# Kernel optimization log

Measured on AMD Instinct MI355X. Metric: run time of the kernel, lower is better.

Reference implementation:

```python
import jax, jax.numpy as jnp
import numpy as np

B, S, DIM, H, DH, FF = 2, 2048, 2048, 16, 128, 8192
EPS = 1e-6


def rmsnorm(x, g):
    xf = x.astype(jnp.float32)
    y = xf * jax.lax.rsqrt(jnp.mean(xf * xf, axis=-1, keepdims=True) + EPS)
    return y.astype(x.dtype) * g


def rope_cache(seq_len, head_dim):
    inv_freq = 1.0 / (10000.0 ** (jnp.arange(0, head_dim, 2, dtype=jnp.float32) / head_dim))
    t = jnp.arange(seq_len, dtype=jnp.float32)
    freqs = jnp.outer(t, inv_freq)              # [S, DH/2]
    emb = jnp.concatenate([freqs, freqs], -1)   # [S, DH]
    return jnp.cos(emb), jnp.sin(emb)


def rotate_half(x):
    x1, x2 = jnp.split(x, 2, axis=-1)
    return jnp.concatenate([-x2, x1], axis=-1)


def apply_rope(x, cos, sin):
    # x: [B,H,S,DH]; cos/sin: [S,DH] broadcast per position
    c = cos[None, None, :, :]
    s = sin[None, None, :, :]
    return x * c + rotate_half(x) * s


def setup_inputs() -> dict:
    key = jax.random.key(0)
    ks = jax.random.split(key, 10)
    std = 0.02
    x = jax.random.normal(ks[0], (B, S, DIM), jnp.float32)
    mask = jnp.tril(jnp.ones((S, S), dtype=bool))[None, None]  # causal [1,1,S,S]
    wq = jax.random.normal(ks[1], (H * DH, DIM), jnp.float32) * std
    wk = jax.random.normal(ks[2], (H * DH, DIM), jnp.float32) * std
    wv = jax.random.normal(ks[3], (H * DH, DIM), jnp.float32) * std
    wo = jax.random.normal(ks[4], (DIM, H * DH), jnp.float32) * std
    w1 = jax.random.normal(ks[5], (FF, DIM), jnp.float32) * std
    w2 = jax.random.normal(ks[6], (DIM, FF), jnp.float32) * std
    w3 = jax.random.normal(ks[7], (FF, DIM), jnp.float32) * std
    g_attn = jnp.ones((DIM,), jnp.float32)
    g_ffn = jnp.ones((DIM,), jnp.float32)
    return {"x": x, "mask": mask, "wq": wq, "wk": wk, "wv": wv, "wo": wo,
            "w1": w1, "w2": w2, "w3": w3, "g_attn": g_attn, "g_ffn": g_ffn}


def reference(x, mask, wq, wk, wv, wo, w1, w2, w3, g_attn, g_ffn):
    b, s, _ = x.shape
    scale = 1.0 / np.sqrt(DH)
    # --- attention sublayer ---
    h = rmsnorm(x, g_attn)
    q = jnp.einsum('bsd,ed->bse', h, wq).reshape(b, s, H, DH).transpose(0, 2, 1, 3)
    k = jnp.einsum('bsd,ed->bse', h, wk).reshape(b, s, H, DH).transpose(0, 2, 1, 3)
    v = jnp.einsum('bsd,ed->bse', h, wv).reshape(b, s, H, DH).transpose(0, 2, 1, 3)
    cos, sin = rope_cache(s, DH)
    q = apply_rope(q, cos, sin)
    k = apply_rope(k, cos, sin)
    scores = jnp.einsum('bhqd,bhkd->bhqk', q, k) * scale
    scores = jnp.where(mask, scores, -1e9)
    attn = jax.nn.softmax(scores, axis=-1)
    o = jnp.einsum('bhqk,bhkd->bhqd', attn, v)
    o = o.transpose(0, 2, 1, 3).reshape(b, s, H * DH)
    x = x + jnp.einsum('bse,de->bsd', o, wo)
    # --- SwiGLU FFN sublayer ---
    h2 = rmsnorm(x, g_ffn)
    u = jnp.einsum('bsd,fd->bsf', h2, w1)
    g = jnp.einsum('bsd,fd->bsf', h2, w3)
    ff = jnp.einsum('bsf,df->bsd', jax.nn.silu(u) * g, w2)
    return x + ff
```

## Files before the change

kernel.cpp:

```cpp
#include <hip/hip_runtime.h>
#include <hip/hip_bf16.h>
#include <math.h>

typedef __hip_bfloat16 bf16;
typedef short short8 __attribute__((ext_vector_type(8)));
typedef float f32x4 __attribute__((ext_vector_type(4)));

#define Bq 2
#define Sq 2048
#define Dq 2048
#define Hq 16
#define DHq 128
#define FFq 8192
#define Mq 4096

__device__ __forceinline__ float b2f(bf16 x) { return __bfloat162float(x); }
__device__ __forceinline__ bf16 f2b(float x) { return __float2bfloat16(x); }

__device__ __forceinline__ void gload16(const void* g, void* lds_base) {
  __builtin_amdgcn_global_load_lds(
      (const __attribute__((address_space(1))) void*)g,
      (__attribute__((address_space(3))) void*)lds_base,
      16, 0, 0);
}

__global__ __launch_bounds__(256)
void conv_k(const float* __restrict__ src, bf16* __restrict__ dst, long n) {
  const long stride = (long)gridDim.x * 256 * 8;
  for (long i = ((long)blockIdx.x * 256 + threadIdx.x) * 8; i < n; i += stride) {
    f32x4 a = *(const f32x4*)(src + i);
    f32x4 b = *(const f32x4*)(src + i + 4);
    union { short8 s; bf16 h[8]; } u;
#pragma unroll
    for (int j = 0; j < 4; ++j) { u.h[j] = f2b(a[j]); u.h[j + 4] = f2b(b[j]); }
    *(short8*)(dst + i) = u.s;
  }
}

#define BAR8() { asm volatile("" ::: "memory"); __builtin_amdgcn_s_barrier(); asm volatile("" ::: "memory"); }
#define VMC4() { asm volatile("s_waitcnt vmcnt(4)" ::: "memory"); __builtin_amdgcn_sched_barrier(0); }

#define STG8(Gp, ldX, rowOff, kt, XsBuf)                                        \
  gload16(Gp + (size_t)((rowOff) + w8 + lr) * (size_t)(ldX) + (kt) + sCol,      \
          &XsBuf[(rowOff) + w8][0]);                                            \
  gload16(Gp + (size_t)((rowOff) + 64 + w8 + lr) * (size_t)(ldX) + (kt) + sCol, \
          &XsBuf[(rowOff) + 64 + w8][0]);

#define RD_A8(dst, XsBuf, mb)                                                   \
  _Pragma("unroll") for (int mi = 0; mi < 4; ++mi) {                            \
    const int ra = wmBase + ((mb) + mi) * 16 + c;                               \
    _Pragma("unroll") for (int kk = 0; kk < 2; ++kk)                            \
      dst[mi][kk] = *(const short8*)&XsBuf[ra][(((kk * 4 + g) ^ (ra & 7)) << 3)]; \
  }

#define RD_B8(dst, XsBuf, nb_)                                                  \
  _Pragma("unroll") for (int ni = 0; ni < 2; ++ni) {                            \
    const int rb = wnBase + ((nb_) + ni) * 16 + c;                              \
    _Pragma("unroll") for (int kk = 0; kk < 2; ++kk)                            \
      dst[ni][kk] = *(const short8*)&XsBuf[rb][(((kk * 4 + g) ^ (rb & 7)) << 3)]; \
  }

#define MFMA_Q8(afv, bfv, mb, nb_)                                              \
  __builtin_amdgcn_s_setprio(1);                                                \
  _Pragma("unroll") for (int mi = 0; mi < 4; ++mi)                              \
    _Pragma("unroll") for (int ni = 0; ni < 2; ++ni)                            \
      _Pragma("unroll") for (int kk = 0; kk < 2; ++kk)                          \
        acc[(mb) + mi][(nb_) + ni] = __builtin_amdgcn_mfma_f32_16x16x32_bf16(   \
            afv[mi][kk], bfv[ni][kk], acc[(mb) + mi][(nb_) + ni], 0, 0, 0);     \
  __builtin_amdgcn_s_setprio(0);

template <int EPI>
__global__ __launch_bounds__(512, 2)
void gemm8(const bf16* __restrict__ A, const bf16* __restrict__ Bt,
           const void* __restrict__ R, void* __restrict__ C,
           int N, int K, int ldb, long long boff) {
  __shared__ __align__(16) bf16 As[2][256][64];
  __shared__ __align__(16) bf16 Bs[2][256][64];
  const int tid = threadIdx.x;
  const int w = tid >> 6, l = tid & 63;
  const int g = l >> 4, c = l & 15;
  const int w8 = w * 8, lr = l >> 3;
  const int sCol = (((l & 7) ^ lr) << 3);

  const int nwg = gridDim.x * gridDim.y;
  const int orig = blockIdx.x + blockIdx.y * gridDim.x;
  const int qq = nwg >> 3, rr8 = nwg & 7;
  const int xcd = orig & 7, idx8 = orig >> 3;
  const int wg = (xcd < rr8 ? xcd * (qq + 1) : rr8 * (qq + 1) + (xcd - rr8) * qq) + idx8;
  const int bm = (wg / gridDim.x) * 256;
  const int bn = (wg % gridDim.x) * 256;

  const int wmBase = (w >> 2) * 128;
  const int wnBase = (w & 3) * 64;

  const bf16* Ab = A + (size_t)bm * K;
  const bf16* Bb = Bt + (size_t)bn * ldb + (size_t)boff;

  f32x4 acc[8][4] = {};
  const int nt = K >> 6;

  STG8(Ab, K, 0, 0, As[0]); STG8(Ab, K, 128, 0, As[0]);
  STG8(Bb, ldb, 0, 0, Bs[0]); STG8(Bb, ldb, 128, 0, Bs[0]);
  STG8(Bb, ldb, 0, 64, Bs[1]); STG8(Bb, ldb, 128, 64, Bs[1]);
  VMC4(); BAR8();

  short8 af[4][2], af2[4][2], bf[2][2], bf2[2][2];
  for (int it = 0; it < (nt >> 1); ++it) {
    const int t = it * 2;
    const int kt1 = (t + 1) << 6;
    const int kt2 = (t + 2 < nt ? t + 2 : nt - 1) << 6;
    const int kt3 = (t + 3 < nt ? t + 3 : nt - 1) << 6;
    RD_A8(af, As[0], 0); RD_B8(bf, Bs[0], 0); RD_B8(bf2, Bs[0], 2);
    STG8(Ab, K, 0, kt1, As[1]); STG8(Ab, K, 128, kt1, As[1]);
    BAR8();
    MFMA_Q8(af, bf, 0, 0); MFMA_Q8(af, bf2, 0, 2);
    BAR8();
    RD_A8(af2, As[0], 4);
    STG8(Bb, ldb, 0, kt2, Bs[0]); STG8(Bb, ldb, 128, kt2, Bs[0]);
    BAR8();
    MFMA_Q8(af2, bf, 4, 0); MFMA_Q8(af2, bf2, 4, 2);
    VMC4(); BAR8();
    RD_A8(af, As[1], 0); RD_B8(bf, Bs[1], 0); RD_B8(bf2, Bs[1], 2);
    STG8(Ab, K, 0, kt2, As[0]); STG8(Ab, K, 128, kt2, As[0]);
    BAR8();
    MFMA_Q8(af, bf, 0, 0); MFMA_Q8(af, bf2, 0, 2);
    BAR8();
    RD_A8(af2, As[1], 4);
    STG8(Bb, ldb, 0, kt3, Bs[1]); STG8(Bb, ldb, 128, kt3, Bs[1]);
    BAR8();
    MFMA_Q8(af2, bf, 4, 0); MFMA_Q8(af2, bf2, 4, 2);
    VMC4(); BAR8();
  }

  const int rbase = bm + wmBase + g * 4;
  const int cbase = bn + wnBase + c;
#pragma unroll
  for (int m = 0; m < 8; ++m)
#pragma unroll
    for (int r = 0; r < 4; ++r) {
      const int row = rbase + m * 16 + r;
#pragma unroll
      for (int n = 0; n < 4; ++n) {
        const size_t idx = (size_t)row * N + (cbase + n * 16);
        float vacc = acc[m][n][r];
        if (EPI == 1) {
          ((float*)C)[idx] = vacc + ((const float*)R)[idx];
        } else if (EPI == 2) {
          const float u = b2f(((const bf16*)R)[idx]);
          ((bf16*)C)[idx] = f2b((u / (1.f + expf(-u))) * vacc);
        } else {
          ((bf16*)C)[idx] = f2b(vacc);
        }
      }
    }
}

template <int EPI>
__global__ __launch_bounds__(256)
void gemm3(const bf16* __restrict__ A, const bf16* __restrict__ Bt,
           const void* __restrict__ R, void* __restrict__ C,
           int N, int K, int ldb, long long boff) {
  __shared__ __align__(16) bf16 As[128][64];
  __shared__ __align__(16) bf16 Bs[128][64];
  const int tid = threadIdx.x;
  const int w = tid >> 6;
  const int l = tid & 63;

  const int nwg = gridDim.x * gridDim.y;
  const int orig = blockIdx.x + blockIdx.y * gridDim.x;
  const int qq = nwg >> 3, rr8 = nwg & 7;
  const int xcd = orig & 7, idx8 = orig >> 3;
  const int wg = (xcd < rr8 ? xcd * (qq + 1) : rr8 * (qq + 1) + (xcd - rr8) * qq) + idx8;
  const int bm = (wg / gridDim.x) * 128;
  const int bn = (wg % gridDim.x) * 128;

  const int wr = (w >> 1) * 64;
  const int wc = (w & 1) * 64;
  f32x4 acc[4][4] = {};

  const bf16* Ab = A + (size_t)bm * K;
  const bf16* Bb = Bt + (size_t)bn * ldb + (size_t)boff;

  const int sRow = w * 8 + (l >> 3);
  const int sCol = (((l & 7) ^ (l >> 3)) << 3);

  for (int kt = 0; kt < K; kt += 64) {
    __syncthreads();
#pragma unroll
    for (int i = 0; i < 4; ++i) {
      gload16(Ab + (size_t)(i * 32 + sRow) * K + kt + sCol, &As[i * 32 + w * 8][0]);
      gload16(Bb + (size_t)(i * 32 + sRow) * ldb + kt + sCol, &Bs[i * 32 + w * 8][0]);
    }
    __syncthreads();

#pragma unroll
    for (int kk = 0; kk < 2; ++kk) {
      short8 af[4], bfv[4];
#pragma unroll
      for (int m = 0; m < 4; ++m) {
        const int ra = wr + m * 16 + (l & 15);
        af[m] = *(const short8*)&As[ra][(((kk * 4 + (l >> 4)) ^ (ra & 7)) << 3)];
      }
#pragma unroll
      for (int n = 0; n < 4; ++n) {
        const int rb = wc + n * 16 + (l & 15);
        bfv[n] = *(const short8*)&Bs[rb][(((kk * 4 + (l >> 4)) ^ (rb & 7)) << 3)];
      }
#pragma unroll
      for (int m = 0; m < 4; ++m)
#pragma unroll
        for (int n = 0; n < 4; ++n)
          acc[m][n] = __builtin_amdgcn_mfma_f32_16x16x32_bf16(af[m], bfv[n], acc[m][n], 0, 0, 0);
    }
  }

  const int rbase = bm + wr + (l >> 4) * 4;
  const int cbase = bn + wc + (l & 15);
#pragma unroll
  for (int m = 0; m < 4; ++m)
#pragma unroll
    for (int r = 0; r < 4; ++r) {
      const int row = rbase + m * 16 + r;
#pragma unroll
      for (int n = 0; n < 4; ++n) {
        const size_t idx = (size_t)row * N + (cbase + n * 16);
        float vacc = acc[m][n][r];
        if (EPI == 1) {
          ((float*)C)[idx] = vacc + ((const float*)R)[idx];
        } else if (EPI == 2) {
          const float u = b2f(((const bf16*)R)[idx]);
          ((bf16*)C)[idx] = f2b((u / (1.f + expf(-u))) * vacc);
        } else {
          ((bf16*)C)[idx] = f2b(vacc);
        }
      }
    }
}

template <int EPI>
__global__ __launch_bounds__(256)
void gemm2(const bf16* __restrict__ A, const float* __restrict__ Bt,
           const void* __restrict__ R, void* __restrict__ C,
           int N, int K, int ldb, long long boff) {
  __shared__ __align__(16) bf16 As[128][64];
  __shared__ __align__(16) float Bsf[128][64];
  const int tid = threadIdx.x;
  const int w = tid >> 6;
  const int l = tid & 63;

  const int nwg = gridDim.x * gridDim.y;
  const int orig = blockIdx.x + blockIdx.y * gridDim.x;
  const int qq = nwg >> 3, rr8 = nwg & 7;
  const int xcd = orig & 7, idx8 = orig >> 3;
  const int wg = (xcd < rr8 ? xcd * (qq + 1) : rr8 * (qq + 1) + (xcd - rr8) * qq) + idx8;
  const int bm = (wg / gridDim.x) * 128;
  const int bn = (wg % gridDim.x) * 128;

  const int wr = (w >> 1) * 64;
  const int wc = (w & 1) * 64;
  f32x4 acc[4][4] = {};

  const bf16* Ab = A + (size_t)bm * K;
  const float* Bb = Bt + (size_t)bn * ldb + (size_t)boff;

  const int aSrcCol = (((l & 7) ^ (l >> 3)) << 3);
  const int bKey = (w * 4 + (l >> 4)) & 7;
  const int bSrcCol = (((l & 15) ^ bKey) << 2);

  for (int kt = 0; kt < K; kt += 64) {
    __syncthreads();
#pragma unroll
    for (int i = 0; i < 4; ++i)
      gload16(Ab + (size_t)(i * 32 + w * 8 + (l >> 3)) * K + kt + aSrcCol,
              &As[i * 32 + w * 8][0]);
#pragma unroll
    for (int i = 0; i < 8; ++i)
      gload16(Bb + (size_t)(i * 16 + w * 4 + (l >> 4)) * ldb + kt + bSrcCol,
              &Bsf[i * 16 + w * 4][0]);
    __syncthreads();

#pragma unroll
    for (int kk = 0; kk < 2; ++kk) {
      short8 af[4], bfv[4];
#pragma unroll
      for (int m = 0; m < 4; ++m) {
        const int ra = wr + m * 16 + (l & 15);
        const int pb = (kk * 4 + (l >> 4)) ^ (ra & 7);
        af[m] = *(const short8*)&As[ra][pb * 8];
      }
#pragma unroll
      for (int n = 0; n < 4; ++n) {
        const int rb = wc + n * 16 + (l & 15);
        const int b0 = kk * 8 + (l >> 4) * 2;
        const f32x4 x0 = *(const f32x4*)&Bsf[rb][(b0 ^ (rb & 7)) * 4];
        const f32x4 x1 = *(const f32x4*)&Bsf[rb][((b0 + 1) ^ (rb & 7)) * 4];
        union { short8 s; bf16 h[8]; } u;
#pragma unroll
        for (int j = 0; j < 4; ++j) { u.h[j] = f2b(x0[j]); u.h[j + 4] = f2b(x1[j]); }
        bfv[n] = u.s;
      }
#pragma unroll
      for (int m = 0; m < 4; ++m)
#pragma unroll
        for (int n = 0; n < 4; ++n)
          acc[m][n] = __builtin_amdgcn_mfma_f32_16x16x32_bf16(af[m], bfv[n], acc[m][n], 0, 0, 0);
    }
  }

  const int rbase = bm + wr + (l >> 4) * 4;
  const int cbase = bn + wc + (l & 15);
#pragma unroll
  for (int m = 0; m < 4; ++m)
#pragma unroll
    for (int r = 0; r < 4; ++r) {
      const int row = rbase + m * 16 + r;
#pragma unroll
      for (int n = 0; n < 4; ++n) {
        const size_t idx = (size_t)row * N + (cbase + n * 16);
        float vacc = acc[m][n][r];
        if (EPI == 1) {
          ((float*)C)[idx] = vacc + ((const float*)R)[idx];
        } else if (EPI == 2) {
          const float u = b2f(((const bf16*)R)[idx]);
          ((bf16*)C)[idx] = f2b((u / (1.f + expf(-u))) * vacc);
        } else {
          ((bf16*)C)[idx] = f2b(vacc);
        }
      }
    }
}

__global__ __launch_bounds__(256)
void rmsnorm_k(const float* __restrict__ xin, const float* __restrict__ g,
               bf16* __restrict__ out) {
  const int row = blockIdx.x;
  const int tid = threadIdx.x;
  const float* xp = xin + (size_t)row * Dq + tid * 8;
  f32x4 a = *(const f32x4*)xp, b = *(const f32x4*)(xp + 4);
  float xf[8];
#pragma unroll
  for (int j = 0; j < 4; ++j) { xf[j] = a[j]; xf[j + 4] = b[j]; }
  float ss = 0.f;
#pragma unroll
  for (int j = 0; j < 8; ++j) ss += xf[j] * xf[j];
#pragma unroll
  for (int off = 32; off > 0; off >>= 1) ss += __shfl_down(ss, off);
  __shared__ float red[4];
  if ((tid & 63) == 0) red[tid >> 6] = ss;
  __syncthreads();
  const float rms = rsqrtf((red[0] + red[1] + red[2] + red[3]) * (1.f / (float)Dq) + 1e-6f);
  const float* gp = g + tid * 8;
  f32x4 ga = *(const f32x4*)gp, gb = *(const f32x4*)(gp + 4);
  union { short8 s; bf16 h[8]; } uo;
#pragma unroll
  for (int j = 0; j < 4; ++j) {
    uo.h[j] = f2b(xf[j] * rms * ga[j]);
    uo.h[j + 4] = f2b(xf[j + 4] * rms * gb[j]);
  }
  *(short8*)(out + (size_t)row * Dq + tid * 8) = uo.s;
}

__global__ __launch_bounds__(256)
void rope_k(bf16* __restrict__ q, bf16* __restrict__ k, int ld) {
  const size_t idx = (size_t)blockIdx.x * 256 + threadIdx.x;
  const int i = (int)(idx & 63);
  const int h = (int)((idx >> 6) & 15);
  const int s = (int)((idx >> 10) & 2047);
  const int b = (int)(idx >> 21);
  const float f = (float)s * powf(10000.f, -(float)i * (1.f / 64.f));
  float sn, cs;
  sincosf(f, &sn, &cs);
  const size_t base = ((size_t)(b * Sq + s)) * ld + h * DHq + i;
  const float qa = b2f(q[base]), qb_ = b2f(q[base + 64]);
  q[base] = f2b(qa * cs - qb_ * sn);
  q[base + 64] = f2b(qb_ * cs + qa * sn);
  const float ka = b2f(k[base]), kb_ = b2f(k[base + 64]);
  k[base] = f2b(ka * cs - kb_ * sn);
  k[base + 64] = f2b(kb_ * cs + ka * sn);
}

__device__ __forceinline__ int swz8(int row) { return (((row >> 3) ^ row) & 7) << 3; }

#define ATTN_COMPUTE(AQ, QB, QROW, M_, L_, OACC, KV0, CUR)                        \
  {                                                                               \
    f32x4 sc[4] = {};                                                             \
    __builtin_amdgcn_s_setprio(1);                                                \
    _Pragma("unroll") for (int n = 0; n < 4; ++n) {                               \
      const int krow = n * 16 + c;                                                \
      const int sw = swz8(krow);                                                  \
      _Pragma("unroll") for (int kk = 0; kk < 4; ++kk) {                          \
        short8 ak = *(const short8*)&Ks[CUR][krow][(kk * 32 + g * 8) ^ sw];       \
        sc[n] = __builtin_amdgcn_mfma_f32_16x16x32_bf16(ak, AQ[kk], sc[n], 0, 0, 0); \
      }                                                                           \
    }                                                                             \
    __builtin_amdgcn_s_setprio(0);                                                \
    float p[4][4];                                                                \
    float tmax = -3.0e38f;                                                        \
    if ((KV0) + 63 <= (QB)) {                                                     \
      _Pragma("unroll") for (int n = 0; n < 4; ++n)                               \
        _Pragma("unroll") for (int r = 0; r < 4; ++r) {                           \
          const float val = sc[n][r] * SCALE;                                     \
          p[n][r] = val;                                                          \
          tmax = fmaxf(tmax, val);                                                \
        }                                                                         \
    } else {                                                                      \
      _Pragma("unroll") for (int n = 0; n < 4; ++n)                               \
        _Pragma("unroll") for (int r = 0; r < 4; ++r) {                           \
          const int kvg = (KV0) + n * 16 + g * 4 + r;                             \
          float val = sc[n][r] * SCALE;                                           \
          if (kvg > (QROW)) val = -3.0e38f;                                       \
          p[n][r] = val;                                                          \
          tmax = fmaxf(tmax, val);                                                \
        }                                                                         \
    }                                                                             \
    tmax = fmaxf(tmax, __shfl_xor(tmax, 16));                                     \
    tmax = fmaxf(tmax, __shfl_xor(tmax, 32));                                     \
    const bool grow = !__all(tmax <= M_);                                         \
    const float m_new = grow ? fmaxf(M_, tmax) : M_;                              \
    float tsum = 0.f;                                                             \
    _Pragma("unroll") for (int n = 0; n < 4; ++n)                                 \
      _Pragma("unroll") for (int r = 0; r < 4; ++r) {                             \
        const float pv = expf(p[n][r] - m_new);                                   \
        p[n][r] = pv;                                                             \
        tsum += pv;                                                               \
      }                                                                           \
    tsum += __shfl_xor(tsum, 16);                                                 \
    tsum += __shfl_xor(tsum, 32);                                                 \
    if (grow) {                                                                   \
      const float corr = expf(M_ - m_new);                                        \
      L_ = L_ * corr + tsum;                                                      \
      M_ = m_new;                                                                 \
      _Pragma("unroll") for (int dt = 0; dt < 8; ++dt) OACC[dt] *= corr;          \
    } else {                                                                      \
      L_ += tsum;                                                                 \
    }                                                                             \
    const int keyc = (c ^ (c >> 3)) & 7;                                          \
    _Pragma("unroll") for (int n = 0; n < 4; ++n) {                               \
      union { unsigned long long u; bf16 hh[4]; } pk;                             \
      _Pragma("unroll") for (int r = 0; r < 4; ++r) pk.hh[r] = f2b(p[n][r]);      \
      const int blk = (2 * n + (g >> 1)) ^ keyc;                                  \
      *(unsigned long long*)&Ps[w][c][blk * 8 + (g & 1) * 4] = pk.u;              \
    }                                                                             \
    short8 ap[2];                                                                 \
    _Pragma("unroll") for (int kk = 0; kk < 2; ++kk)                              \
      ap[kk] = *(const short8*)&Ps[w][c][(kk * 32 + g * 8) ^ (keyc << 3)];        \
    __builtin_amdgcn_s_setprio(1);                                                \
    _Pragma("unroll") for (int dt = 0; dt < 8; ++dt) {                            \
      const int vrow = dt * 16 + c;                                               \
      const int vsw = swz8(vrow);                                                 \
      _Pragma("unroll") for (int kk = 0; kk < 2; ++kk) {                          \
        short8 av = *(const short8*)&Vt[CUR][vrow][(kk * 32 + g * 8) ^ vsw];      \
        OACC[dt] = __builtin_amdgcn_mfma_f32_16x16x32_bf16(av, ap[kk], OACC[dt], 0, 0, 0); \
      }                                                                           \
    }                                                                             \
    __builtin_amdgcn_s_setprio(0);                                                \
  }

__global__ __launch_bounds__(512)
void attn_k(const bf16* __restrict__ q, const bf16* __restrict__ k,
            const bf16* __restrict__ v, bf16* __restrict__ o, int ld) {
  __shared__ __align__(16) bf16 Ks[2][64][128];
  __shared__ __align__(16) bf16 Vt[2][128][64];
  __shared__ __align__(16) bf16 Ps[8][16][64];
  const int tid = threadIdx.x;
  const int w = tid >> 6, l = tid & 63;
  const int g = l >> 4, c = l & 15;
  const int x = blockIdx.x;
  const int h = blockIdx.y;
  const int b = blockIdx.z;
  const size_t hoff = (size_t)h * DHq;
  const float SCALE = 0.08838834764831845f;

  const int q0h = (15 - x) * 128, q0l = x * 128;
  const int qbh = q0h + w * 16, qbl = q0l + w * 16;
  const int qrh = qbh + c, qrl = qbl + c;

  short8 aqh[4], aql[4];
  {
    const bf16* qph = q + (size_t)(b * Sq + qrh) * ld + hoff + g * 8;
    const bf16* qpl = q + (size_t)(b * Sq + qrl) * ld + hoff + g * 8;
#pragma unroll
    for (int kk = 0; kk < 4; ++kk) {
      aqh[kk] = *(const short8*)(qph + kk * 32);
      aql[kk] = *(const short8*)(qpl + kk * 32);
    }
  }

  float mh = -3.0e38f, lh = 0.f, ml = -3.0e38f, ll_ = 0.f;
  f32x4 oh[8] = {}, ol[8] = {};

  const int stRow = tid >> 4;
  const int stBlk = tid & 15;
  const int ntiles = (q0h >> 6) + 2;

  {
#pragma unroll
    for (int i = 0; i < 2; ++i) {
      const int kr = i * 32 + w * 4 + (l >> 4);
      const int key = (kr ^ (kr >> 3)) & 7;
      gload16(k + (size_t)(b * Sq + kr) * ld + hoff + ((c ^ key) << 3),
              &Ks[0][i * 32 + w * 4][0]);
    }
    const int c0 = stBlk * 8;
#pragma unroll
    for (int i = 0; i < 2; ++i) {
      const int vr = i * 32 + stRow;
      union { short8 s; bf16 hh[8]; } uv;
      uv.s = *(const short8*)(v + (size_t)(b * Sq + vr) * ld + hoff + c0);
#pragma unroll
      for (int j = 0; j < 8; ++j) Vt[0][c0 + j][vr ^ swz8(c0 + j)] = uv.hh[j];
    }
  }
  __syncthreads();

  for (int t = 0; t < ntiles; ++t) {
    const int cur = t & 1, nxt = cur ^ 1;
    const int kv0 = t * 64;
    const bool pf = (t + 1 < ntiles);
    short8 vpa, vpb;
    if (pf) {
      const int kvn = kv0 + 64;
#pragma unroll
      for (int i = 0; i < 2; ++i) {
        const int kr = i * 32 + w * 4 + (l >> 4);
        const int key = (kr ^ (kr >> 3)) & 7;
        gload16(k + (size_t)(b * Sq + kvn + kr) * ld + hoff + ((c ^ key) << 3),
                &Ks[nxt][i * 32 + w * 4][0]);
      }
      vpa = *(const short8*)(v + (size_t)(b * Sq + kvn + stRow) * ld + hoff + stBlk * 8);
      vpb = *(const short8*)(v + (size_t)(b * Sq + kvn + 32 + stRow) * ld + hoff + stBlk * 8);
    }

    if (kv0 <= qbh + 15) ATTN_COMPUTE(aqh, qbh, qrh, mh, lh, oh, kv0, cur);

    if (pf) {
      const int c0 = stBlk * 8;
      union { short8 s; bf16 hh[8]; } uv;
      uv.s = vpa;
#pragma unroll
      for (int j = 0; j < 8; ++j) Vt[nxt][c0 + j][stRow ^ swz8(c0 + j)] = uv.hh[j];
      uv.s = vpb;
#pragma unroll
      for (int j = 0; j < 8; ++j) Vt[nxt][c0 + j][(32 + stRow) ^ swz8(c0 + j)] = uv.hh[j];
    }

    if (kv0 <= qbl + 15) ATTN_COMPUTE(aql, qbl, qrl, ml, ll_, ol, kv0, cur);

    __syncthreads();
  }

  {
    const float inv = 1.f / lh;
    bf16* op = o + (size_t)(b * Sq + qrh) * Dq + hoff + g * 4;
#pragma unroll
    for (int dt = 0; dt < 8; ++dt) {
      union { unsigned long long u; bf16 hh[4]; } pk;
#pragma unroll
      for (int r = 0; r < 4; ++r) pk.hh[r] = f2b(oh[dt][r] * inv);
      *(unsigned long long*)(op + dt * 16) = pk.u;
    }
  }
  {
    const float inv = 1.f / ll_;
    bf16* op = o + (size_t)(b * Sq + qrl) * Dq + hoff + g * 4;
#pragma unroll
    for (int dt = 0; dt < 8; ++dt) {
      union { unsigned long long u; bf16 hh[4]; } pk;
#pragma unroll
      for (int r = 0; r < 4; ++r) pk.hh[r] = f2b(ol[dt][r] * inv);
      *(unsigned long long*)(op + dt * 16) = pk.u;
    }
  }
}

extern "C" void kernel_launch(void* const* d_in, const int* in_sizes, int n_in,
                              void* d_out, int out_size, void* d_ws, size_t ws_size,
                              hipStream_t stream) {
  (void)in_sizes; (void)n_in; (void)out_size;
  const float* x  = (const float*)d_in[0];
  const float* wq = (const float*)d_in[2];
  const float* wk = (const float*)d_in[3];
  const float* wv = (const float*)d_in[4];
  const float* wo = (const float*)d_in[5];
  const float* w1 = (const float*)d_in[6];
  const float* w2 = (const float*)d_in[7];
  const float* w3 = (const float*)d_in[8];
  const float* ga = (const float*)d_in[9];
  const float* gf = (const float*)d_in[10];
  float* out = (float*)d_out;

  char* ws = (char*)d_ws;
  dim3 blk(256);
  dim3 gA(8, Hq, Bq);
  dim3 blkA(512);
  dim3 blk8(512);

  const size_t SZ_H   = (size_t)Mq * Dq * 2;
  const size_t SZ_QKV = (size_t)Mq * 3 * Dq * 2;
  const size_t SZ_W4  = (size_t)Dq * Dq * 2;
  const size_t SZ_W13 = (size_t)FFq * Dq * 2;
  const size_t ACT    = SZ_H + SZ_QKV;
  const size_t WTS    = 3 * SZ_W4 + SZ_W4 + 3 * SZ_W13;
  const size_t NEED   = ACT + WTS;

  if (ws_size >= NEED) {
    bf16* h    = (bf16*)(ws);
    bf16* qkv  = (bf16*)(ws + SZ_H);
    bf16* ob   = h;
    bf16* h2   = qkv;
    bf16* ub   = (bf16*)(ws + SZ_H + SZ_H);
    char* wb   = ws + ACT;
    bf16* wqkv_b = (bf16*)(wb);
    bf16* wo_b   = (bf16*)(wb + 3 * SZ_W4);
    bf16* w1_b   = (bf16*)(wb + 4 * SZ_W4);
    bf16* w3_b   = (bf16*)(wb + 4 * SZ_W4 + SZ_W13);
    bf16* w2_b   = (bf16*)(wb + 4 * SZ_W4 + 2 * SZ_W13);

    const long nW4 = (long)Dq * Dq, nW13 = (long)FFq * Dq;
    conv_k<<<1024, blk, 0, stream>>>(wq, wqkv_b, nW4);
    conv_k<<<1024, blk, 0, stream>>>(wk, wqkv_b + nW4, nW4);
    conv_k<<<1024, blk, 0, stream>>>(wv, wqkv_b + 2 * nW4, nW4);
    conv_k<<<1024, blk, 0, stream>>>(wo, wo_b, nW4);
    conv_k<<<2048, blk, 0, stream>>>(w1, w1_b, nW13);
    conv_k<<<2048, blk, 0, stream>>>(w3, w3_b, nW13);
    conv_k<<<2048, blk, 0, stream>>>(w2, w2_b, nW13);

    rmsnorm_k<<<Mq, blk, 0, stream>>>(x, ga, h);
    gemm3<0><<<dim3(48, 32), blk, 0, stream>>>(h, wqkv_b, nullptr, qkv, 6144, Dq, Dq, 0);
    rope_k<<<(Bq * Sq * Hq * 64) / 256, blk, 0, stream>>>(qkv, qkv + Dq, 3 * Dq);
    attn_k<<<gA, blkA, 0, stream>>>(qkv, qkv + Dq, qkv + 2 * Dq, ob, 3 * Dq);
    gemm3<1><<<dim3(16, 32), blk, 0, stream>>>(ob, wo_b, x, out, Dq, Dq, Dq, 0);
    rmsnorm_k<<<Mq, blk, 0, stream>>>(out, gf, h2);
    for (int hh = 0; hh < 2; ++hh) {
      bf16* w1h = w1_b + (size_t)hh * 4096 * Dq;
      bf16* w3h = w3_b + (size_t)hh * 4096 * Dq;
      gemm8<0><<<dim3(16, 16), blk8, 0, stream>>>(h2, w1h, nullptr, ub, 4096, Dq, Dq, 0);
      gemm8<2><<<dim3(16, 16), blk8, 0, stream>>>(h2, w3h, ub, ub, 4096, Dq, Dq, 0);
      gemm3<1><<<dim3(16, 32), blk, 0, stream>>>(ub, w2_b, out, out, Dq, 4096, FFq,
                                                 (long long)hh * 4096);
    }
  } else {
    const size_t MS = (size_t)Mq * Dq * 2;
    bf16* h  = (bf16*)(ws);
    bf16* kb = (bf16*)(ws + MS);
    bf16* vb = (bf16*)(ws + 2 * MS);
    bf16* qb = (bf16*)(ws + 3 * MS);
    bf16* ub = (bf16*)(ws);
    bf16* ob = h;
    bf16* h2 = qb;

    dim3 gD(Dq / 128, Mq / 128);
    dim3 gU(32, Mq / 128);

    rmsnorm_k<<<Mq, blk, 0, stream>>>(x, ga, h);
    gemm2<0><<<gD, blk, 0, stream>>>(h, wq, nullptr, qb, Dq, Dq, Dq, 0);
    gemm2<0><<<gD, blk, 0, stream>>>(h, wk, nullptr, kb, Dq, Dq, Dq, 0);
    gemm2<0><<<gD, blk, 0, stream>>>(h, wv, nullptr, vb, Dq, Dq, Dq, 0);
    rope_k<<<(Bq * Sq * Hq * 64) / 256, blk, 0, stream>>>(qb, kb, Dq);
    attn_k<<<gA, blkA, 0, stream>>>(qb, kb, vb, ob, Dq);
    gemm2<1><<<gD, blk, 0, stream>>>(ob, wo, x, out, Dq, Dq, Dq, 0);
    rmsnorm_k<<<Mq, blk, 0, stream>>>(out, gf, h2);
    for (int hh = 0; hh < 2; ++hh) {
      const long long bo13 = (long long)hh * 4096 * 2048;
      gemm2<0><<<gU, blk, 0, stream>>>(h2, w1, nullptr, ub, 4096, Dq, Dq, bo13);
      gemm2<2><<<gU, blk, 0, stream>>>(h2, w3, ub, ub, 4096, Dq, Dq, bo13);
      gemm2<1><<<gD, blk, 0, stream>>>(ub, w2, out, out, Dq, 4096, FFq,
                                       (long long)hh * 4096);
    }
  }
}
```

Before: 891.9 us.

## Replace single-buffered GEMM with double-buffered 128x256 tile, 8-wave kernel

Replaces the 128x128, 4-wave, single-buffered gemm3 with gemm12: a 512-thread kernel using 128x256 output tiles and double-buffered LDS. Async global-to-LDS loads for the next K tiles are interleaved with MFMA half-phases, gated by vmcnt waits, barriers and setprio. The aim is to hide load latency behind compute and raise arithmetic intensity for the QKV, output-projection and W2 GEMMs. In exchange it uses more LDS and many barriers, and its correctness depends on the ping-pong ordering and the clamped prefetch indices at the tail.

```diff
diff --git a/kernel.cpp b/kernel.cpp
--- a/kernel.cpp
+++ b/kernel.cpp
@@ -39,6 +39,7 @@
 
 #define BAR8() { asm volatile("" ::: "memory"); __builtin_amdgcn_s_barrier(); asm volatile("" ::: "memory"); }
 #define VMC4() { asm volatile("s_waitcnt vmcnt(4)" ::: "memory"); __builtin_amdgcn_sched_barrier(0); }
+#define VMC2() { asm volatile("s_waitcnt vmcnt(2)" ::: "memory"); __builtin_amdgcn_sched_barrier(0); }
 
 #define STG8(Gp, ldX, rowOff, kt, XsBuf)                                        \
   gload16(Gp + (size_t)((rowOff) + w8 + lr) * (size_t)(ldX) + (kt) + sCol,      \
@@ -155,16 +156,41 @@
     }
 }
 
+#define RD_A12(dst, XsBuf)                                                      \
+  _Pragma("unroll") for (int mi = 0; mi < 4; ++mi) {                            \
+    const int ra = wmB12 + mi * 16 + c;                                         \
+    _Pragma("unroll") for (int kk = 0; kk < 2; ++kk)                            \
+      dst[mi][kk] = *(const short8*)&XsBuf[ra][(((kk * 4 + g) ^ (ra & 7)) << 3)]; \
+  }
+
+#define RD_B12(dst, XsBuf, nb_)                                                 \
+  _Pragma("unroll") for (int ni = 0; ni < 2; ++ni) {                            \
+    const int rb = wnB12 + ((nb_) + ni) * 16 + c;                               \
+    _Pragma("unroll") for (int kk = 0; kk < 2; ++kk)                            \
+      dst[ni][kk] = *(const short8*)&XsBuf[rb][(((kk * 4 + g) ^ (rb & 7)) << 3)]; \
+  }
+
+#define MFMA_H12(afv, bfv, nb_)                                                 \
+  __builtin_amdgcn_s_setprio(1);                                                \
+  _Pragma("unroll") for (int mi = 0; mi < 4; ++mi)                              \
+    _Pragma("unroll") for (int ni = 0; ni < 2; ++ni)                            \
+      _Pragma("unroll") for (int kk = 0; kk < 2; ++kk)                          \
+        acc[mi][(nb_) + ni] = __builtin_amdgcn_mfma_f32_16x16x32_bf16(          \
+            afv[mi][kk], bfv[ni][kk], acc[mi][(nb_) + ni], 0, 0, 0);            \
+  __builtin_amdgcn_s_setprio(0);
+
 template <int EPI>
-__global__ __launch_bounds__(256)
-void gemm3(const bf16* __restrict__ A, const bf16* __restrict__ Bt,
-           const void* __restrict__ R, void* __restrict__ C,
-           int N, int K, int ldb, long long boff) {
-  __shared__ __align__(16) bf16 As[128][64];
-  __shared__ __align__(16) bf16 Bs[128][64];
+__global__ __launch_bounds__(512, 2)
+void gemm12(const bf16* __restrict__ A, const bf16* __restrict__ Bt,
+            const void* __restrict__ R, void* __restrict__ C,
+            int N, int K, int ldb, long long boff) {
+  __shared__ __align__(16) bf16 As[2][128][64];
+  __shared__ __align__(16) bf16 Bs[2][256][64];
   const int tid = threadIdx.x;
-  const int w = tid >> 6;
-  const int l = tid & 63;
+  const int w = tid >> 6, l = tid & 63;
+  const int g = l >> 4, c = l & 15;
+  const int w8 = w * 8, lr = l >> 3;
+  const int sCol = (((l & 7) ^ lr) << 3);
 
   const int nwg = gridDim.x * gridDim.y;
   const int orig = blockIdx.x + blockIdx.y * gridDim.x;
@@ -172,50 +198,52 @@
   const int xcd = orig & 7, idx8 = orig >> 3;
   const int wg = (xcd < rr8 ? xcd * (qq + 1) : rr8 * (qq + 1) + (xcd - rr8) * qq) + idx8;
   const int bm = (wg / gridDim.x) * 128;
-  const int bn = (wg % gridDim.x) * 128;
-
-  const int wr = (w >> 1) * 64;
-  const int wc = (w & 1) * 64;
-  f32x4 acc[4][4] = {};
+  const int bn = (wg % gridDim.x) * 256;
+
+  const int wmB12 = (w >> 2) * 64;
+  const int wnB12 = (w & 3) * 64;
 
   const bf16* Ab = A + (size_t)bm * K;
   const bf16* Bb = Bt + (size_t)bn * ldb + (size_t)boff;
 
-  const int sRow = w * 8 + (l >> 3);
-  const int sCol = (((l & 7) ^ (l >> 3)) << 3);
-
-  for (int kt = 0; kt < K; kt += 64) {
-    __syncthreads();
-#pragma unroll
-    for (int i = 0; i < 4; ++i) {
-      gload16(Ab + (size_t)(i * 32 + sRow) * K + kt + sCol, &As[i * 32 + w * 8][0]);
-      gload16(Bb + (size_t)(i * 32 + sRow) * ldb + kt + sCol, &Bs[i * 32 + w * 8][0]);
-    }
-    __syncthreads();
-
-#pragma unroll
-    for (int kk = 0; kk < 2; ++kk) {
-      short8 af[4], bfv[4];
-#pragma unroll
-      for (int m = 0; m < 4; ++m) {
-        const int ra = wr + m * 16 + (l & 15);
-        af[m] = *(const short8*)&As[ra][(((kk * 4 + (l >> 4)) ^ (ra & 7)) << 3)];
-      }
-#pragma unroll
-      for (int n = 0; n < 4; ++n) {
-        const int rb = wc + n * 16 + (l & 15);
-        bfv[n] = *(const short8*)&Bs[rb][(((kk * 4 + (l >> 4)) ^ (rb & 7)) << 3)];
-      }
-#pragma unroll
-      for (int m = 0; m < 4; ++m)
-#pragma unroll
-        for (int n = 0; n < 4; ++n)
-          acc[m][n] = __builtin_amdgcn_mfma_f32_16x16x32_bf16(af[m], bfv[n], acc[m][n], 0, 0, 0);
-    }
-  }
-
-  const int rbase = bm + wr + (l >> 4) * 4;
-  const int cbase = bn + wc + (l & 15);
+  f32x4 acc[4][4] = {};
+  const int nt = K >> 6;
+
+  STG8(Ab, K, 0, 0, As[0]);
+  STG8(Bb, ldb, 0, 0, Bs[0]); STG8(Bb, ldb, 128, 0, Bs[0]);
+  STG8(Ab, K, 0, 64, As[1]);
+  VMC2(); BAR8();
+
+  short8 af[4][2], af2[4][2], bfa[2][2], bfa2[2][2], bfb[2][2], bfb2[2][2];
+  for (int it = 0; it < (nt >> 1); ++it) {
+    const int t = it * 2;
+    const int kt1 = (t + 1) << 6;
+    const int kt2 = (t + 2 < nt ? t + 2 : nt - 1) << 6;
+    const int kt3 = (t + 3 < nt ? t + 3 : nt - 1) << 6;
+    RD_A12(af, As[0]); RD_B12(bfa, Bs[0], 0);
+    STG8(Bb, ldb, 0, kt1, Bs[1]); STG8(Bb, ldb, 128, kt1, Bs[1]);
+    BAR8();
+    MFMA_H12(af, bfa, 0);
+    BAR8();
+    RD_B12(bfa2, Bs[0], 2);
+    STG8(Ab, K, 0, kt2, As[0]);
+    BAR8();
+    MFMA_H12(af, bfa2, 2);
+    VMC2(); BAR8();
+    RD_A12(af2, As[1]); RD_B12(bfb, Bs[1], 0);
+    STG8(Bb, ldb, 0, kt2, Bs[0]); STG8(Bb, ldb, 128, kt2, Bs[0]);
+    BAR8();
+    MFMA_H12(af2, bfb, 0);
+    BAR8();
+    RD_B12(bfb2, Bs[1], 2);
+    STG8(Ab, K, 0, kt3, As[1]);
+    BAR8();
+    MFMA_H12(af2, bfb2, 2);
+    VMC2(); BAR8();
+  }
+
+  const int rbase = bm + wmB12 + g * 4;
+  const int cbase = bn + wnB12 + c;
 #pragma unroll
   for (int m = 0; m < 4; ++m)
 #pragma unroll
@@ -626,18 +654,18 @@
     conv_k<<<2048, blk, 0, stream>>>(w2, w2_b, nW13);
 
     rmsnorm_k<<<Mq, blk, 0, stream>>>(x, ga, h);
-    gemm3<0><<<dim3(48, 32), blk, 0, stream>>>(h, wqkv_b, nullptr, qkv, 6144, Dq, Dq, 0);
+    gemm12<0><<<dim3(24, 32), blk8, 0, stream>>>(h, wqkv_b, nullptr, qkv, 6144, Dq, Dq, 0);
     rope_k<<<(Bq * Sq * Hq * 64) / 256, blk, 0, stream>>>(qkv, qkv + Dq, 3 * Dq);
     attn_k<<<gA, blkA, 0, stream>>>(qkv, qkv + Dq, qkv + 2 * Dq, ob, 3 * Dq);
-    gemm3<1><<<dim3(16, 32), blk, 0, stream>>>(ob, wo_b, x, out, Dq, Dq, Dq, 0);
+    gemm12<1><<<dim3(8, 32), blk8, 0, stream>>>(ob, wo_b, x, out, Dq, Dq, Dq, 0);
     rmsnorm_k<<<Mq, blk, 0, stream>>>(out, gf, h2);
     for (int hh = 0; hh < 2; ++hh) {
       bf16* w1h = w1_b + (size_t)hh * 4096 * Dq;
       bf16* w3h = w3_b + (size_t)hh * 4096 * Dq;
       gemm8<0><<<dim3(16, 16), blk8, 0, stream>>>(h2, w1h, nullptr, ub, 4096, Dq, Dq, 0);
       gemm8<2><<<dim3(16, 16), blk8, 0, stream>>>(h2, w3h, ub, ub, 4096, Dq, Dq, 0);
-      gemm3<1><<<dim3(16, 32), blk, 0, stream>>>(ub, w2_b, out, out, Dq, 4096, FFq,
-                                                 (long long)hh * 4096);
+      gemm12<1><<<dim3(8, 32), blk8, 0, stream>>>(ub, w2_b, out, out, Dq, 4096, FFq,
+                                                  (long long)hh * 4096);
     }
   } else {
     const size_t MS = (size_t)Mq * Dq * 2;
```

After: 883.3 us. About the same (-1.0%).
